# Performance work log

Hardware: AMD Instinct MI355X
Metric: run time of the kernel (lower is better)

The kernel has to match this reference:

```python
import jax, jax.numpy as jnp
import numpy as np

E = 8          # moe_expert_count
CAPACITY = 1024  # per-expert capacity C = S / E (capacity factor 1)


def _top1_gate(features, wg):
    """Top-1 gate with capacity, returning combine_weights [S,E,C],
    dispatch_mask [S,E,C], and load-balancing aux loss (standard Switch/BASE-style gate
    matching the (l_aux, combine_weights, dispatch_mask) interface used by BaseLayer)."""
    S, M = features.shape
    logits = features @ wg                      # [S, E]
    gates = jax.nn.softmax(logits, axis=-1)     # [S, E]
    idx = jnp.argmax(gates, axis=-1)            # [S] expert assignment
    mask1 = jax.nn.one_hot(idx, E, dtype=features.dtype)  # [S, E]
    # position of each token inside its expert's buffer (0-based, order of arrival)
    locations = jnp.cumsum(mask1, axis=0) - mask1          # [S, E]
    loc = jnp.sum(locations * mask1, axis=1).astype(jnp.int32)  # [S]
    keep = (loc < CAPACITY).astype(features.dtype)          # drop overflow tokens
    mask1 = mask1 * keep[:, None]
    gate_s = jnp.sum(gates * mask1, axis=1)                 # [S] gate prob of kept tokens
    loc_oh = jax.nn.one_hot(loc, CAPACITY, dtype=features.dtype)  # [S, C]
    combine = gate_s[:, None, None] * mask1[:, :, None] * loc_oh[:, None, :]  # [S,E,C]
    dispatch = (combine > 0).astype(features.dtype)
    # load-balance aux loss: E * sum(mean_prob_e * frac_tokens_e)
    me = jnp.mean(gates, axis=0)
    ce = jnp.mean(mask1, axis=0)
    l_aux = jnp.sum(me * ce) * E
    return l_aux, combine, dispatch


def setup_inputs() -> dict:
    key = jax.random.key(0)
    k0, k1, k2, k3 = jax.random.split(key, 4)
    B, T, M, H = 4, 2048, 512, 1024
    return {
        "hidden_states": jax.random.normal(k0, (B, T, M), dtype=jnp.float32),
        "wg": jax.random.normal(k1, (M, E), dtype=jnp.float32) * 0.02,
        "w1": jax.random.normal(k2, (E, M, H), dtype=jnp.float32) * 0.02,
        "b1": jnp.zeros((E, H), dtype=jnp.float32),
        "w2": jax.random.normal(k3, (E, H, M), dtype=jnp.float32) * 0.02,
        "b2": jnp.zeros((E, M), dtype=jnp.float32),
    }


def reference(hidden_states, wg, w1, b1, w2, b2):
    B, T, M = hidden_states.shape
    feats = hidden_states.reshape(-1, M)            # [S, M]
    l_aux, combine, dispatch = _top1_gate(feats, wg)
    # dense one-hot dispatch matmul: (E*C, S) @ (S, M) -> [E, C, M]
    dispatched = jnp.einsum('sec,sm->ecm', dispatch, feats)
    # per-expert FFN (BaseSublayer: Linear -> ReLU -> Linear)
    h = jax.nn.relu(jnp.einsum('ecm,emh->ech', dispatched, w1) + b1[:, None, :])
    expert_out = jnp.einsum('ech,ehn->ecn', h, w2) + b2[:, None, :]  # [E, C, M]
    # dense combine matmul: (S, E*C) @ (E*C, M) -> [S, M]
    combined = jnp.einsum('sec,ecn->sn', combine, expert_out)
    return combined.reshape(B, T, -1), l_aux
```

## Files before the change

### kernel.cpp

```cpp
#include <hip/hip_runtime.h>

#define S_TOK 8192
#define M_DIM 512
#define E_NUM 8
#define CAP   1024
#define H_DIM 1024
#define NGATE_BLK (S_TOK / 4)

typedef __attribute__((ext_vector_type(8))) short bf16x8;
typedef __attribute__((ext_vector_type(4))) float f32x4;

__device__ static inline unsigned short f2bf(float f) {
    unsigned int u = __float_as_uint(f);
    unsigned int r = (u + 0x7fffu + ((u >> 16) & 1u)) >> 16;
    return (unsigned short)r;
}

__device__ static inline void async_copy16(const void* g, void* l) {
    __builtin_amdgcn_global_load_lds(
        (const __attribute__((address_space(1))) void*)g,
        (__attribute__((address_space(3))) void*)l, 16, 0, 0);
}

__global__ __launch_bounds__(256) void gate_kernel(
    const float* __restrict__ feats, const float* __restrict__ wg,
    int* __restrict__ idx, float* __restrict__ gate_top,
    float* __restrict__ gates_psum, unsigned short* __restrict__ xb)
{
    __shared__ float gsh[4][8];
    const int wave = threadIdx.x >> 6;
    const int lane = threadIdx.x & 63;
    const int s = blockIdx.x * 4 + wave;

    const float* xrow = feats + (size_t)s * M_DIM;
    const int m0 = lane * 8;

    const float4 va = *(const float4*)(xrow + m0);
    const float4 vb = *(const float4*)(xrow + m0 + 4);
    float xv[8] = {va.x, va.y, va.z, va.w, vb.x, vb.y, vb.z, vb.w};

    {
        bf16x8 o;
#pragma unroll
        for (int j = 0; j < 8; ++j) o[j] = (short)f2bf(xv[j]);
        *(bf16x8*)(xb + (size_t)s * M_DIM + m0) = o;
        if (blockIdx.x == 0 && wave == 0) {
            bf16x8 z = (bf16x8){0,0,0,0,0,0,0,0};
            *(bf16x8*)(xb + (size_t)S_TOK * M_DIM + m0) = z;
        }
    }

    float p[8];
#pragma unroll
    for (int e = 0; e < 8; ++e) p[e] = 0.f;
#pragma unroll
    for (int j = 0; j < 8; ++j) {
        const float4 wa = *(const float4*)(wg + (m0 + j) * 8);
        const float4 wb2 = *(const float4*)(wg + (m0 + j) * 8 + 4);
        const float x = xv[j];
        p[0] += x * wa.x;  p[1] += x * wa.y;  p[2] += x * wa.z;  p[3] += x * wa.w;
        p[4] += x * wb2.x; p[5] += x * wb2.y; p[6] += x * wb2.z; p[7] += x * wb2.w;
    }
#pragma unroll
    for (int e = 0; e < 8; ++e) {
        float v = p[e];
#pragma unroll
        for (int off = 1; off < 64; off <<= 1) v += __shfl_xor(v, off, 64);
        p[e] = v;
    }
    if (lane == 0) {
        float mx = p[0];
#pragma unroll
        for (int e = 1; e < 8; ++e) mx = fmaxf(mx, p[e]);
        float ex[8], sum = 0.f;
#pragma unroll
        for (int e = 0; e < 8; ++e) { ex[e] = expf(p[e] - mx); sum += ex[e]; }
        const float inv = 1.0f / sum;
        int best = 0; float bl = p[0];
#pragma unroll
        for (int e = 1; e < 8; ++e) { if (p[e] > bl) { bl = p[e]; best = e; } }
#pragma unroll
        for (int e = 0; e < 8; ++e) gsh[wave][e] = ex[e] * inv;
        idx[s] = best;
        gate_top[s] = ex[best] * inv;
    }
    __syncthreads();
    if (threadIdx.x < 8) {
        const int e = threadIdx.x;
        gates_psum[blockIdx.x * 8 + e] =
            gsh[0][e] + gsh[1][e] + gsh[2][e] + gsh[3][e];
    }
}

__global__ __launch_bounds__(256) void scan_kernel(
    const int* __restrict__ idx, const float* __restrict__ gate_top,
    const float* __restrict__ gates_psum,
    float* __restrict__ gate_final, int* __restrict__ token_list,
    int* __restrict__ kept, float* __restrict__ laux,
    int* __restrict__ dropped, int* __restrict__ ndrop)
{
    __shared__ int   cnts[256][8];
    __shared__ float msum[256][8];
    __shared__ int   totals[8];
    __shared__ float mesum[8];
    __shared__ int   dropctr;

    const int t = threadIdx.x;
    const int base = t * 32;

    for (int i = t; i < E_NUM * CAP; i += 256) token_list[i] = S_TOK;
    if (t == 0) dropctr = 0;

    int c[8];
#pragma unroll
    for (int e = 0; e < 8; ++e) c[e] = 0;
    for (int i = 0; i < 32; ++i) {
        const int ei = idx[base + i];
#pragma unroll
        for (int e = 0; e < 8; ++e) c[e] += (ei == e) ? 1 : 0;
    }

    float g[8];
#pragma unroll
    for (int e = 0; e < 8; ++e) g[e] = 0.f;
    for (int i = 0; i < NGATE_BLK / 256; ++i) {
        const float* gp = gates_psum + (size_t)(t + 256 * i) * 8;
        const float4 a = *(const float4*)gp;
        const float4 b = *(const float4*)(gp + 4);
        g[0] += a.x; g[1] += a.y; g[2] += a.z; g[3] += a.w;
        g[4] += b.x; g[5] += b.y; g[6] += b.z; g[7] += b.w;
    }
#pragma unroll
    for (int e = 0; e < 8; ++e) { cnts[t][e] = c[e]; msum[t][e] = g[e]; }
    __syncthreads();

    if (t < 8) {
        int run = 0; float ms = 0.f;
        for (int r = 0; r < 256; ++r) {
            const int v = cnts[r][t];
            cnts[r][t] = run;
            run += v;
            ms += msum[r][t];
        }
        totals[t] = run;
        mesum[t] = ms;
        kept[t] = run < CAP ? run : CAP;
    }
    __syncthreads();

    if (t == 0) {
        float l = 0.f;
        for (int e = 0; e < 8; ++e) {
            const int ke = totals[e] < CAP ? totals[e] : CAP;
            l += (mesum[e] / (float)S_TOK) * ((float)ke / (float)S_TOK);
        }
        laux[0] = l * (float)E_NUM;
    }

    int rc[8];
#pragma unroll
    for (int e = 0; e < 8; ++e) rc[e] = cnts[t][e];

    for (int i = 0; i < 32; ++i) {
        const int s = base + i;
        const int ei = idx[s];
        int loc = 0;
#pragma unroll
        for (int e = 0; e < 8; ++e) {
            if (ei == e) { loc = rc[e]; rc[e] = rc[e] + 1; }
        }
        const bool keepit = loc < CAP;
        gate_final[s] = keepit ? gate_top[s] : 0.f;
        if (keepit) {
            token_list[ei * CAP + loc] = s;
        } else {
            const int d = atomicAdd(&dropctr, 1);
            dropped[d] = s;
        }
    }
    __syncthreads();
    if (t == 0) ndrop[0] = dropctr;
}

__global__ __launch_bounds__(256) void zero_dropped(
    const int* __restrict__ dropped, const int* __restrict__ ndrop,
    float* __restrict__ out)
{
    const int n = ndrop[0];
    const int t = threadIdx.x;
    for (int d = blockIdx.x; d < n; d += gridDim.x) {
        const int s = dropped[d];
        *(float2*)(out + (size_t)s * M_DIM + t * 2) = make_float2(0.f, 0.f);
    }
}

__global__ __launch_bounds__(256) void convert_w(
    const float* __restrict__ w1, unsigned short* __restrict__ w1t,
    const float* __restrict__ w2, unsigned short* __restrict__ w2t)
{
    __shared__ float tile[32][33];
    int b = blockIdx.x;
    const float* src; unsigned short* dst;
    int e, k0, n0, K, N;
    if (b < 4096) {
        e = b >> 9; k0 = ((b >> 5) & 15) * 32; n0 = (b & 31) * 32;
        K = 512; N = 1024; src = w1; dst = w1t;
    } else {
        b -= 4096;
        e = b >> 9; k0 = ((b >> 4) & 31) * 32; n0 = (b & 15) * 32;
        K = 1024; N = 512; src = w2; dst = w2t;
    }
    const int t = threadIdx.x;
    const int r = t >> 3, c4 = (t & 7) * 4;
    {
        const float4 v = *(const float4*)(src + ((size_t)e * K + k0 + r) * N + n0 + c4);
        tile[r][c4 + 0] = v.x; tile[r][c4 + 1] = v.y;
        tile[r][c4 + 2] = v.z; tile[r][c4 + 3] = v.w;
    }
    __syncthreads();
    {
        ushort4 o;
        o.x = f2bf(tile[c4 + 0][r]); o.y = f2bf(tile[c4 + 1][r]);
        o.z = f2bf(tile[c4 + 2][r]); o.w = f2bf(tile[c4 + 3][r]);
        *(ushort4*)(dst + ((size_t)e * N + n0 + r) * K + k0 + c4) = o;
    }
}

__global__ __launch_bounds__(256) void ffn1_mfma(
    const unsigned short* __restrict__ xb, const unsigned short* __restrict__ w1t,
    const float* __restrict__ b1, const int* __restrict__ tok,
    const int* __restrict__ kept, unsigned short* __restrict__ h)
{
    const int b = blockIdx.x;
    const int e = b & 7;
    const int r = b >> 3;
    const int ct = r >> 3, nt = r & 7;
    const int c0 = ct * 128, n0 = nt * 128;
    if (c0 >= kept[e]) return;

    __shared__ __align__(16) short Alds[2][128 * 64];
    __shared__ __align__(16) short Blds[2][128 * 64];
    __shared__ int srow[128];

    const int t = threadIdx.x;
    const int wave = t >> 6, lane = t & 63;
    const int wm = wave & 1, wn = wave >> 1;
    const int q = lane >> 4, lr = lane & 15;

    if (t < 128) srow[t] = tok[e * CAP + c0 + t];

    auto stage = [&](int buf, int kb) {
#pragma unroll
        for (int i = 0; i < 4; ++i) {
            const int lin = (i * 4 + wave) * 64 + lane;
            const int row = lin >> 3;
            const int ch = (lin & 7) ^ (row & 7);
            async_copy16(xb + (size_t)srow[row] * M_DIM + kb + ch * 8,
                         &Alds[buf][lin * 8]);
        }
#pragma unroll
        for (int i = 0; i < 4; ++i) {
            const int lin = (i * 4 + wave) * 64 + lane;
            const int row = lin >> 3;
            const int ch = (lin & 7) ^ (row & 7);
            async_copy16(w1t + ((size_t)e * H_DIM + n0 + row) * M_DIM + kb + ch * 8,
                         &Blds[buf][lin * 8]);
        }
    };

    f32x4 acc[4][4];
#pragma unroll
    for (int mi = 0; mi < 4; ++mi)
#pragma unroll
        for (int ni = 0; ni < 4; ++ni) acc[mi][ni] = (f32x4){0.f, 0.f, 0.f, 0.f};

    __syncthreads();
    stage(0, 0);

    int cur = 0;
    for (int kb = 0; kb < M_DIM; kb += 64) {
        __syncthreads();
        if (kb + 64 < M_DIM) stage(cur ^ 1, kb + 64);

#pragma unroll
        for (int kk = 0; kk < 64; kk += 32) {
            const int cb = kk >> 3;
            bf16x8 af[4], bfv[4];
#pragma unroll
            for (int mi = 0; mi < 4; ++mi) {
                const int R = wm * 64 + mi * 16 + lr;
                af[mi] = *(const bf16x8*)(&Alds[cur][(R * 8 + ((cb + q) ^ (R & 7))) * 8]);
            }
#pragma unroll
            for (int ni = 0; ni < 4; ++ni) {
                const int R = wn * 64 + ni * 16 + lr;
                bfv[ni] = *(const bf16x8*)(&Blds[cur][(R * 8 + ((cb + q) ^ (R & 7))) * 8]);
            }
#pragma unroll
            for (int mi = 0; mi < 4; ++mi)
#pragma unroll
                for (int ni = 0; ni < 4; ++ni)
                    acc[mi][ni] = __builtin_amdgcn_mfma_f32_16x16x32_bf16(
                        af[mi], bfv[ni], acc[mi][ni], 0, 0, 0);
        }
        cur ^= 1;
    }

#pragma unroll
    for (int ni = 0; ni < 4; ++ni) {
        const int col = n0 + wn * 64 + ni * 16 + lr;
        const float bias = b1[e * H_DIM + col];
#pragma unroll
        for (int mi = 0; mi < 4; ++mi) {
            const int rowl = wm * 64 + mi * 16 + q * 4;
            const size_t basep = (size_t)(e * CAP + c0 + rowl) * H_DIM + col;
#pragma unroll
            for (int r2 = 0; r2 < 4; ++r2) {
                const float v = fmaxf(acc[mi][ni][r2] + bias, 0.f);
                h[basep + (size_t)r2 * H_DIM] = f2bf(v);
            }
        }
    }
}

__global__ __launch_bounds__(256) void ffn2_mfma(
    const unsigned short* __restrict__ h, const unsigned short* __restrict__ w2t,
    const float* __restrict__ b2, const int* __restrict__ tok,
    const int* __restrict__ kept, const float* __restrict__ gate_final,
    float* __restrict__ out)
{
    const int b = blockIdx.x;
    const int e = b & 7;
    const int r = b >> 3;
    const int ct = r >> 3, nt = r & 7;
    const int c0 = ct * 128, n0 = nt * 64;
    if (c0 >= kept[e]) return;

    __shared__ __align__(16) short Alds[2][128 * 64];
    __shared__ __align__(16) short Blds[2][64 * 64];
    __shared__ int   stok[128];
    __shared__ float sgf[128];

    const int t = threadIdx.x;
    const int wave = t >> 6, lane = t & 63;
    const int wm = wave & 1, wn = wave >> 1;
    const int q = lane >> 4, lr = lane & 15;

    if (t < 128) {
        const int tk = tok[e * CAP + c0 + t];
        stok[t] = tk;
        sgf[t] = (tk != S_TOK) ? gate_final[tk] : 0.f;
    }

    auto stage = [&](int buf, int kb) {
#pragma unroll
        for (int i = 0; i < 4; ++i) {
            const int lin = (i * 4 + wave) * 64 + lane;
            const int row = lin >> 3;
            const int ch = (lin & 7) ^ (row & 7);
            async_copy16(h + (size_t)(e * CAP + c0 + row) * H_DIM + kb + ch * 8,
                         &Alds[buf][lin * 8]);
        }
#pragma unroll
        for (int i = 0; i < 2; ++i) {
            const int lin = (i * 4 + wave) * 64 + lane;
            const int row = lin >> 3;
            const int ch = (lin & 7) ^ (row & 7);
            async_copy16(w2t + ((size_t)e * M_DIM + n0 + row) * H_DIM + kb + ch * 8,
                         &Blds[buf][lin * 8]);
        }
    };

    f32x4 acc[4][2];
#pragma unroll
    for (int mi = 0; mi < 4; ++mi)
#pragma unroll
        for (int ni = 0; ni < 2; ++ni) acc[mi][ni] = (f32x4){0.f, 0.f, 0.f, 0.f};

    __syncthreads();
    stage(0, 0);

    int cur = 0;
    for (int kb = 0; kb < H_DIM; kb += 64) {
        __syncthreads();
        if (kb + 64 < H_DIM) stage(cur ^ 1, kb + 64);

#pragma unroll
        for (int kk = 0; kk < 64; kk += 32) {
            const int cb = kk >> 3;
            bf16x8 af[4], bfv[2];
#pragma unroll
            for (int mi = 0; mi < 4; ++mi) {
                const int R = wm * 64 + mi * 16 + lr;
                af[mi] = *(const bf16x8*)(&Alds[cur][(R * 8 + ((cb + q) ^ (R & 7))) * 8]);
            }
#pragma unroll
            for (int ni = 0; ni < 2; ++ni) {
                const int R = wn * 32 + ni * 16 + lr;
                bfv[ni] = *(const bf16x8*)(&Blds[cur][(R * 8 + ((cb + q) ^ (R & 7))) * 8]);
            }
#pragma unroll
            for (int mi = 0; mi < 4; ++mi)
#pragma unroll
                for (int ni = 0; ni < 2; ++ni)
                    acc[mi][ni] = __builtin_amdgcn_mfma_f32_16x16x32_bf16(
                        af[mi], bfv[ni], acc[mi][ni], 0, 0, 0);
        }
        cur ^= 1;
    }

#pragma unroll
    for (int ni = 0; ni < 2; ++ni) {
        const int col = n0 + wn * 32 + ni * 16 + lr;
        const float bias = b2[e * M_DIM + col];
#pragma unroll
        for (int mi = 0; mi < 4; ++mi) {
            const int rowl = wm * 64 + mi * 16 + q * 4;
#pragma unroll
            for (int r2 = 0; r2 < 4; ++r2) {
                const int slot = rowl + r2;
                const int tokid = stok[slot];
                if (tokid != S_TOK) {
                    out[(size_t)tokid * M_DIM + col] = sgf[slot] * (acc[mi][ni][r2] + bias);
                }
            }
        }
    }
}

extern "C" void kernel_launch(void* const* d_in, const int* in_sizes, int n_in,
                              void* d_out, int out_size, void* d_ws, size_t ws_size,
                              hipStream_t stream) {
    const float* feats = (const float*)d_in[0];
    const float* wg    = (const float*)d_in[1];
    const float* w1    = (const float*)d_in[2];
    const float* b1    = (const float*)d_in[3];
    const float* w2    = (const float*)d_in[4];
    const float* b2    = (const float*)d_in[5];
    float* out = (float*)d_out;

    char* ws = (char*)d_ws;
    size_t off = 0;
    unsigned short* h   = (unsigned short*)(ws + off); off += (size_t)E_NUM * CAP * H_DIM * 2;
    unsigned short* xb  = (unsigned short*)(ws + off); off += (size_t)(S_TOK + 1) * M_DIM * 2;
    unsigned short* w1t = (unsigned short*)(ws + off); off += (size_t)E_NUM * H_DIM * M_DIM * 2;
    unsigned short* w2t = (unsigned short*)(ws + off); off += (size_t)E_NUM * M_DIM * H_DIM * 2;
    int*   idx        = (int*)(ws + off);   off += (size_t)S_TOK * 4;
    float* gate_top   = (float*)(ws + off); off += (size_t)S_TOK * 4;
    float* gate_final = (float*)(ws + off); off += (size_t)S_TOK * 4;
    float* gates_psum = (float*)(ws + off); off += (size_t)NGATE_BLK * 8 * 4;
    int*   token_list = (int*)(ws + off);   off += (size_t)S_TOK * 4;
    int*   dropped    = (int*)(ws + off);   off += (size_t)S_TOK * 4;
    int*   kept       = (int*)(ws + off);   off += 64;
    int*   ndrop      = (int*)(ws + off);   off += 64;
    (void)ws_size; (void)n_in; (void)in_sizes;

    gate_kernel<<<NGATE_BLK, 256, 0, stream>>>(feats, wg, idx, gate_top,
                                               gates_psum, xb);
    convert_w<<<8192, 256, 0, stream>>>(w1, w1t, w2, w2t);
    scan_kernel<<<1, 256, 0, stream>>>(idx, gate_top, gates_psum, gate_final,
                                       token_list, kept, out + (size_t)S_TOK * M_DIM,
                                       dropped, ndrop);
    zero_dropped<<<256, 256, 0, stream>>>(dropped, ndrop, out);
    ffn1_mfma<<<512, 256, 0, stream>>>(xb, w1t, b1, token_list, kept, h);
    ffn2_mfma<<<512, 256, 0, stream>>>(h, w2t, b2, token_list, kept,
                                       gate_final, out);
}
```

Baseline: 186.1 us.

## Parallelize scan with wave shuffles, fold drop-zeroing into scan, retile ffn2

The single-block scan now does its per-expert prefix sums and gate-mean reductions with wave shuffles instead of eight serial threads walking 256 rows. Zeroing of dropped tokens moves into the scan kernel using a shared-memory list, which removes one kernel launch. ffn2 switches from 128-row double-buffered tiles to 64-row single-buffered tiles on twice as many blocks, trading copy/compute overlap for more parallelism and fewer idle tiles. A single block now zeroes all dropped rows serially, which could be slow when many tokens are dropped.

```diff
diff --git a/kernel.cpp b/kernel.cpp
--- a/kernel.cpp
+++ b/kernel.cpp
@@ -96,16 +96,16 @@
     const int* __restrict__ idx, const float* __restrict__ gate_top,
     const float* __restrict__ gates_psum,
     float* __restrict__ gate_final, int* __restrict__ token_list,
-    int* __restrict__ kept, float* __restrict__ laux,
-    int* __restrict__ dropped, int* __restrict__ ndrop)
+    int* __restrict__ kept, float* __restrict__ out)
 {
-    __shared__ int   cnts[256][8];
-    __shared__ float msum[256][8];
+    __shared__ int   cnts[256][9];
+    __shared__ float wpart[4][8];
     __shared__ int   totals[8];
-    __shared__ float mesum[8];
+    __shared__ int   sdrop[7168];
     __shared__ int   dropctr;
 
     const int t = threadIdx.x;
+    const int wv = t >> 6, ln = t & 63;
     const int base = t * 32;
 
     for (int i = t; i < E_NUM * CAP; i += 256) token_list[i] = S_TOK;
@@ -119,7 +119,6 @@
 #pragma unroll
         for (int e = 0; e < 8; ++e) c[e] += (ei == e) ? 1 : 0;
     }
-
     float g[8];
 #pragma unroll
     for (int e = 0; e < 8; ++e) g[e] = 0.f;
@@ -131,30 +130,48 @@
         g[4] += b.x; g[5] += b.y; g[6] += b.z; g[7] += b.w;
     }
 #pragma unroll
-    for (int e = 0; e < 8; ++e) { cnts[t][e] = c[e]; msum[t][e] = g[e]; }
-    __syncthreads();
-
-    if (t < 8) {
-        int run = 0; float ms = 0.f;
-        for (int r = 0; r < 256; ++r) {
-            const int v = cnts[r][t];
-            cnts[r][t] = run;
-            run += v;
-            ms += msum[r][t];
-        }
-        totals[t] = run;
-        mesum[t] = ms;
-        kept[t] = run < CAP ? run : CAP;
+    for (int e = 0; e < 8; ++e) cnts[t][e] = c[e];
+#pragma unroll
+    for (int e = 0; e < 8; ++e) {
+        float v = g[e];
+#pragma unroll
+        for (int off = 1; off < 64; off <<= 1) v += __shfl_xor(v, off, 64);
+        if (ln == 0) wpart[wv][e] = v;
+    }
+    __syncthreads();
+
+#pragma unroll
+    for (int ee = 0; ee < 2; ++ee) {
+        const int e = wv * 2 + ee;
+        int off = 0;
+#pragma unroll
+        for (int seg = 0; seg < 4; ++seg) {
+            const int r = seg * 64 + ln;
+            const int v = cnts[r][e];
+            int incl = v;
+#pragma unroll
+            for (int d = 1; d < 64; d <<= 1) {
+                const int nn = __shfl_up(incl, d, 64);
+                if (ln >= d) incl += nn;
+            }
+            cnts[r][e] = incl - v + off;
+            off += __shfl(incl, 63, 64);
+        }
+        if (ln == 0) {
+            totals[e] = off;
+            kept[e] = off < CAP ? off : CAP;
+        }
     }
     __syncthreads();
 
     if (t == 0) {
         float l = 0.f;
         for (int e = 0; e < 8; ++e) {
+            const float ms = wpart[0][e] + wpart[1][e] + wpart[2][e] + wpart[3][e];
             const int ke = totals[e] < CAP ? totals[e] : CAP;
-            l += (mesum[e] / (float)S_TOK) * ((float)ke / (float)S_TOK);
-        }
-        laux[0] = l * (float)E_NUM;
+            l += (ms / (float)S_TOK) * ((float)ke / (float)S_TOK);
+        }
+        out[(size_t)S_TOK * M_DIM] = l * (float)E_NUM;
     }
 
     int rc[8];
@@ -175,21 +192,14 @@
             token_list[ei * CAP + loc] = s;
         } else {
             const int d = atomicAdd(&dropctr, 1);
-            dropped[d] = s;
-        }
-    }
-    __syncthreads();
-    if (t == 0) ndrop[0] = dropctr;
-}
-
-__global__ __launch_bounds__(256) void zero_dropped(
-    const int* __restrict__ dropped, const int* __restrict__ ndrop,
-    float* __restrict__ out)
-{
-    const int n = ndrop[0];
-    const int t = threadIdx.x;
-    for (int d = blockIdx.x; d < n; d += gridDim.x) {
-        const int s = dropped[d];
+            sdrop[d] = s;
+        }
+    }
+    __syncthreads();
+
+    const int nd = dropctr;
+    for (int d = 0; d < nd; ++d) {
+        const int s = sdrop[d];
         *(float2*)(out + (size_t)s * M_DIM + t * 2) = make_float2(0.f, 0.f);
     }
 }
@@ -333,33 +343,40 @@
     const int e = b & 7;
     const int r = b >> 3;
     const int ct = r >> 3, nt = r & 7;
-    const int c0 = ct * 128, n0 = nt * 64;
+    const int c0 = ct * 64, n0 = nt * 64;
     if (c0 >= kept[e]) return;
 
-    __shared__ __align__(16) short Alds[2][128 * 64];
-    __shared__ __align__(16) short Blds[2][64 * 64];
-    __shared__ int   stok[128];
-    __shared__ float sgf[128];
+    __shared__ __align__(16) short Alds[64 * 64];
+    __shared__ __align__(16) short Blds[64 * 64];
+    __shared__ int   stok[64];
+    __shared__ float sgf[64];
 
     const int t = threadIdx.x;
     const int wave = t >> 6, lane = t & 63;
     const int wm = wave & 1, wn = wave >> 1;
     const int q = lane >> 4, lr = lane & 15;
 
-    if (t < 128) {
+    if (t < 64) {
         const int tk = tok[e * CAP + c0 + t];
         stok[t] = tk;
         sgf[t] = (tk != S_TOK) ? gate_final[tk] : 0.f;
     }
 
-    auto stage = [&](int buf, int kb) {
-#pragma unroll
-        for (int i = 0; i < 4; ++i) {
+    f32x4 acc[2][2];
+#pragma unroll
+    for (int mi = 0; mi < 2; ++mi)
+#pragma unroll
+        for (int ni = 0; ni < 2; ++ni) acc[mi][ni] = (f32x4){0.f, 0.f, 0.f, 0.f};
+
+    for (int kb = 0; kb < H_DIM; kb += 64) {
+        __syncthreads();
+#pragma unroll
+        for (int i = 0; i < 2; ++i) {
             const int lin = (i * 4 + wave) * 64 + lane;
             const int row = lin >> 3;
             const int ch = (lin & 7) ^ (row & 7);
             async_copy16(h + (size_t)(e * CAP + c0 + row) * H_DIM + kb + ch * 8,
-                         &Alds[buf][lin * 8]);
+                         &Alds[lin * 8]);
         }
 #pragma unroll
         for (int i = 0; i < 2; ++i) {
@@ -367,46 +384,31 @@
             const int row = lin >> 3;
             const int ch = (lin & 7) ^ (row & 7);
             async_copy16(w2t + ((size_t)e * M_DIM + n0 + row) * H_DIM + kb + ch * 8,
-                         &Blds[buf][lin * 8]);
-        }
-    };
-
-    f32x4 acc[4][2];
-#pragma unroll
-    for (int mi = 0; mi < 4; ++mi)
-#pragma unroll
-        for (int ni = 0; ni < 2; ++ni) acc[mi][ni] = (f32x4){0.f, 0.f, 0.f, 0.f};
-
-    __syncthreads();
-    stage(0, 0);
-
-    int cur = 0;
-    for (int kb = 0; kb < H_DIM; kb += 64) {
+                         &Blds[lin * 8]);
+        }
         __syncthreads();
-        if (kb + 64 < H_DIM) stage(cur ^ 1, kb + 64);
 
 #pragma unroll
         for (int kk = 0; kk < 64; kk += 32) {
             const int cb = kk >> 3;
-            bf16x8 af[4], bfv[2];
-#pragma unroll
-            for (int mi = 0; mi < 4; ++mi) {
-                const int R = wm * 64 + mi * 16 + lr;
-                af[mi] = *(const bf16x8*)(&Alds[cur][(R * 8 + ((cb + q) ^ (R & 7))) * 8]);
+            bf16x8 af[2], bfv[2];
+#pragma unroll
+            for (int mi = 0; mi < 2; ++mi) {
+                const int R = wm * 32 + mi * 16 + lr;
+                af[mi] = *(const bf16x8*)(&Alds[(R * 8 + ((cb + q) ^ (R & 7))) * 8]);
             }
 #pragma unroll
             for (int ni = 0; ni < 2; ++ni) {
                 const int R = wn * 32 + ni * 16 + lr;
-                bfv[ni] = *(const bf16x8*)(&Blds[cur][(R * 8 + ((cb + q) ^ (R & 7))) * 8]);
-            }
-#pragma unroll
-            for (int mi = 0; mi < 4; ++mi)
+                bfv[ni] = *(const bf16x8*)(&Blds[(R * 8 + ((cb + q) ^ (R & 7))) * 8]);
+            }
+#pragma unroll
+            for (int mi = 0; mi < 2; ++mi)
 #pragma unroll
                 for (int ni = 0; ni < 2; ++ni)
                     acc[mi][ni] = __builtin_amdgcn_mfma_f32_16x16x32_bf16(
                         af[mi], bfv[ni], acc[mi][ni], 0, 0, 0);
         }
-        cur ^= 1;
     }
 
 #pragma unroll
@@ -414,8 +416,8 @@
         const int col = n0 + wn * 32 + ni * 16 + lr;
         const float bias = b2[e * M_DIM + col];
 #pragma unroll
-        for (int mi = 0; mi < 4; ++mi) {
-            const int rowl = wm * 64 + mi * 16 + q * 4;
+        for (int mi = 0; mi < 2; ++mi) {
+            const int rowl = wm * 32 + mi * 16 + q * 4;
 #pragma unroll
             for (int r2 = 0; r2 < 4; ++r2) {
                 const int slot = rowl + r2;
@@ -450,19 +452,15 @@
     float* gate_final = (float*)(ws + off); off += (size_t)S_TOK * 4;
     float* gates_psum = (float*)(ws + off); off += (size_t)NGATE_BLK * 8 * 4;
     int*   token_list = (int*)(ws + off);   off += (size_t)S_TOK * 4;
-    int*   dropped    = (int*)(ws + off);   off += (size_t)S_TOK * 4;
     int*   kept       = (int*)(ws + off);   off += 64;
-    int*   ndrop      = (int*)(ws + off);   off += 64;
     (void)ws_size; (void)n_in; (void)in_sizes;
 
     gate_kernel<<<NGATE_BLK, 256, 0, stream>>>(feats, wg, idx, gate_top,
                                                gates_psum, xb);
     convert_w<<<8192, 256, 0, stream>>>(w1, w1t, w2, w2t);
     scan_kernel<<<1, 256, 0, stream>>>(idx, gate_top, gates_psum, gate_final,
-                                       token_list, kept, out + (size_t)S_TOK * M_DIM,
-                                       dropped, ndrop);
-    zero_dropped<<<256, 256, 0, stream>>>(dropped, ndrop, out);
+                                       token_list, kept, out);
     ffn1_mfma<<<512, 256, 0, stream>>>(xb, w1t, b1, token_list, kept, h);
-    ffn2_mfma<<<512, 256, 0, stream>>>(h, w2t, b2, token_list, kept,
-                                       gate_final, out);
-}
+    ffn2_mfma<<<1024, 256, 0, stream>>>(h, w2t, b2, token_list, kept,
+                                        gate_final, out);
+}
```

Result: faster. 180.6 us (-3.0%).
